# Kernel optimization log

Measured on AMD Instinct MI355X. Metric: run time of the kernel, lower is better.

Reference implementation:

```python
import jax, jax.numpy as jnp
import numpy as np

# Representation config (from init_kwargs): rep1 = rep2 = degrees [0, 1], mult = 32
N = 50000          # nodes
E = 800000         # edges (avg degree 16)
M = 32             # channel multiplicity (rep2.mult)
L_IN = [0, 1]
L_OUT = [0, 1]
D_IN = sum(2 * l + 1 for l in L_IN)    # 4; rep1_cdims = [0, 1, 4]
D_OUT = sum(2 * l + 1 for l in L_OUT)  # 4
OUT_DIMS = np.array([2 * l + 1 for l in L_OUT])  # [1, 3]


def setup_inputs() -> dict:
    key = jax.random.key(0)
    k1, k2, k3, k4 = jax.random.split(key, 4)
    basis = jax.random.normal(k1, (E, D_OUT, D_IN), dtype=jnp.float32)
    edge_weights = jax.random.normal(k2, (E, len(L_OUT), M), dtype=jnp.float32)
    node_features = jax.random.normal(k3, (N, D_IN, M), dtype=jnp.float32)
    U = jax.random.randint(k4, (E,), 0, N)  # edge source node indices
    return {"basis": basis, "edge_weights": edge_weights,
            "node_features": node_features, "U": U}


def reference(basis, edge_weights, node_features, U):
    # matmulStepOne: gather source-node features per edge, contract with the
    # per-edge equivariant basis (block-structured over rep1 degree slices;
    # equivalent to one dense [D_OUT, D_IN] matmul per edge).
    x = node_features[U]                          # [E, D_IN, M] (irregular gather)
    tmp = jnp.einsum('eoi,eim->eom', basis, x)    # [E, D_OUT, M]
    # matmulStepTwo: degree-wise weighted combine — each output degree block
    # (of size 2l+1) is scaled by its per-edge, per-channel radial weight.
    w = jnp.repeat(edge_weights, OUT_DIMS, axis=1, total_repeat_length=D_OUT)  # [E, D_OUT, M]
    return tmp * w
```

## Files before the change

### kernel.cpp

```cpp
#include <hip/hip_runtime.h>


typedef float f4 __attribute__((ext_vector_type(4)));

__global__ __launch_bounds__(256) void equiv_mm_kernel(
    const float* __restrict__ basis,
    const float* __restrict__ ew,
    const float* __restrict__ nf,
    const int*   __restrict__ U,
    float*       __restrict__ out,
    int E)
{
    int gid = blockIdx.x * blockDim.x + threadIdx.x;
    int e = gid >> 3;
    if (e >= E) return;
    int m0 = (gid & 7) << 2;

    int u = U[e];

    const f4* xp = (const f4*)(nf + (size_t)u * 128 + m0);
    f4 x0 = xp[0];
    f4 x1 = xp[8];
    f4 x2 = xp[16];
    f4 x3 = xp[24];

    const f4* bp = (const f4*)(basis + (size_t)e * 16);
    f4 b0 = bp[0], b1 = bp[1], b2 = bp[2], b3 = bp[3];

    const f4* wp = (const f4*)(ew + (size_t)e * 64 + m0);
    f4 w0 = wp[0];
    f4 w1 = wp[8];

    f4* op = (f4*)(out + (size_t)e * 128 + m0);
    op[0]  = (b0.x * x0 + b0.y * x1 + b0.z * x2 + b0.w * x3) * w0;
    op[8]  = (b1.x * x0 + b1.y * x1 + b1.z * x2 + b1.w * x3) * w1;
    op[16] = (b2.x * x0 + b2.y * x1 + b2.z * x2 + b2.w * x3) * w1;
    op[24] = (b3.x * x0 + b3.y * x1 + b3.z * x2 + b3.w * x3) * w1;
}

extern "C" void kernel_launch(void* const* d_in, const int* in_sizes, int n_in,
                              void* d_out, int out_size, void* d_ws, size_t ws_size,
                              hipStream_t stream) {
    const float* basis = (const float*)d_in[0];
    const float* ew    = (const float*)d_in[1];
    const float* nf    = (const float*)d_in[2];
    const int*   U     = (const int*)d_in[3];
    float* out = (float*)d_out;

    int E = in_sizes[0] / 16;
    long long total = (long long)E * 8;
    int block = 256;
    int grid = (int)((total + block - 1) / block);

    equiv_mm_kernel<<<grid, block, 0, stream>>>(basis, ew, nf, U, out, E);
}
```

Before: 158.0 us.

## Process two edges per thread with grid-stride loop and nontemporal streaming

Each thread now handles two consecutive edges, loading both U indices as one int2 and issuing both node-feature gathers together. The grid is capped at 2048 blocks and threads walk the work with a grid-stride loop. Basis, edge-weight and output accesses use nontemporal loads and stores so streamed data does not evict gathered node features from cache. A one-block tail kernel handles an odd edge count. The changes add register pressure and a second launch when E is odd.

```diff
diff --git a/kernel.cpp b/kernel.cpp
--- a/kernel.cpp
+++ b/kernel.cpp
@@ -9,33 +9,69 @@
     const float* __restrict__ nf,
     const int*   __restrict__ U,
     float*       __restrict__ out,
-    int E)
+    int E, int total)
 {
-    int gid = blockIdx.x * blockDim.x + threadIdx.x;
-    int e = gid >> 3;
-    if (e >= E) return;
-    int m0 = (gid & 7) << 2;
+    const int stride = gridDim.x * blockDim.x;
+    for (int gid = blockIdx.x * blockDim.x + threadIdx.x; gid < total; gid += stride) {
+        int p  = gid >> 3;
+        int m0 = (gid & 7) << 2;
+        int e0 = p << 1;
+        int e1 = e0 + 1;
 
+        int2 uu = ((const int2*)U)[p];
+
+        const f4* xp0 = (const f4*)(nf + (size_t)uu.x * 128 + m0);
+        const f4* xp1 = (const f4*)(nf + (size_t)uu.y * 128 + m0);
+        f4 a0 = xp0[0], a1 = xp0[8], a2 = xp0[16], a3 = xp0[24];
+        f4 c0 = xp1[0], c1 = xp1[8], c2 = xp1[16], c3 = xp1[24];
+
+        const f4* bp0 = (const f4*)(basis + (size_t)e0 * 16);
+        f4 b00 = __builtin_nontemporal_load(bp0 + 0);
+        f4 b01 = __builtin_nontemporal_load(bp0 + 1);
+        f4 b02 = __builtin_nontemporal_load(bp0 + 2);
+        f4 b03 = __builtin_nontemporal_load(bp0 + 3);
+        f4 b10 = __builtin_nontemporal_load(bp0 + 4);
+        f4 b11 = __builtin_nontemporal_load(bp0 + 5);
+        f4 b12 = __builtin_nontemporal_load(bp0 + 6);
+        f4 b13 = __builtin_nontemporal_load(bp0 + 7);
+
+        const f4* wp0 = (const f4*)(ew + (size_t)e0 * 64 + m0);
+        f4 w00 = __builtin_nontemporal_load(wp0 + 0);
+        f4 w01 = __builtin_nontemporal_load(wp0 + 8);
+        f4 w10 = __builtin_nontemporal_load(wp0 + 16);
+        f4 w11 = __builtin_nontemporal_load(wp0 + 24);
+
+        f4* op0 = (f4*)(out + (size_t)e0 * 128 + m0);
+        __builtin_nontemporal_store((b00.x*a0 + b00.y*a1 + b00.z*a2 + b00.w*a3) * w00, op0 + 0);
+        __builtin_nontemporal_store((b01.x*a0 + b01.y*a1 + b01.z*a2 + b01.w*a3) * w01, op0 + 8);
+        __builtin_nontemporal_store((b02.x*a0 + b02.y*a1 + b02.z*a2 + b02.w*a3) * w01, op0 + 16);
+        __builtin_nontemporal_store((b03.x*a0 + b03.y*a1 + b03.z*a2 + b03.w*a3) * w01, op0 + 24);
+        f4* op1 = (f4*)(out + (size_t)e1 * 128 + m0);
+        __builtin_nontemporal_store((b10.x*c0 + b10.y*c1 + b10.z*c2 + b10.w*c3) * w10, op1 + 0);
+        __builtin_nontemporal_store((b11.x*c0 + b11.y*c1 + b11.z*c2 + b11.w*c3) * w11, op1 + 8);
+        __builtin_nontemporal_store((b12.x*c0 + b12.y*c1 + b12.z*c2 + b12.w*c3) * w11, op1 + 16);
+        __builtin_nontemporal_store((b13.x*c0 + b13.y*c1 + b13.z*c2 + b13.w*c3) * w11, op1 + 24);
+    }
+}
+
+__global__ void equiv_mm_tail(
+    const float* __restrict__ basis, const float* __restrict__ ew,
+    const float* __restrict__ nf, const int* __restrict__ U,
+    float* __restrict__ out, int e)
+{
+    int m0 = (threadIdx.x & 7) << 2;
     int u = U[e];
-
     const f4* xp = (const f4*)(nf + (size_t)u * 128 + m0);
-    f4 x0 = xp[0];
-    f4 x1 = xp[8];
-    f4 x2 = xp[16];
-    f4 x3 = xp[24];
-
+    f4 a0 = xp[0], a1 = xp[8], a2 = xp[16], a3 = xp[24];
     const f4* bp = (const f4*)(basis + (size_t)e * 16);
     f4 b0 = bp[0], b1 = bp[1], b2 = bp[2], b3 = bp[3];
-
     const f4* wp = (const f4*)(ew + (size_t)e * 64 + m0);
-    f4 w0 = wp[0];
-    f4 w1 = wp[8];
-
+    f4 w0 = wp[0], w1 = wp[8];
     f4* op = (f4*)(out + (size_t)e * 128 + m0);
-    op[0]  = (b0.x * x0 + b0.y * x1 + b0.z * x2 + b0.w * x3) * w0;
-    op[8]  = (b1.x * x0 + b1.y * x1 + b1.z * x2 + b1.w * x3) * w1;
-    op[16] = (b2.x * x0 + b2.y * x1 + b2.z * x2 + b2.w * x3) * w1;
-    op[24] = (b3.x * x0 + b3.y * x1 + b3.z * x2 + b3.w * x3) * w1;
+    op[0]  = (b0.x*a0 + b0.y*a1 + b0.z*a2 + b0.w*a3) * w0;
+    op[8]  = (b1.x*a0 + b1.y*a1 + b1.z*a2 + b1.w*a3) * w1;
+    op[16] = (b2.x*a0 + b2.y*a1 + b2.z*a2 + b2.w*a3) * w1;
+    op[24] = (b3.x*a0 + b3.y*a1 + b3.z*a2 + b3.w*a3) * w1;
 }
 
 extern "C" void kernel_launch(void* const* d_in, const int* in_sizes, int n_in,
@@ -48,9 +84,13 @@
     float* out = (float*)d_out;
 
     int E = in_sizes[0] / 16;
-    long long total = (long long)E * 8;
+    int pairs = E >> 1;
+    int total = pairs * 8;
     int block = 256;
-    int grid = (int)((total + block - 1) / block);
+    int grid = (total + block - 1) / block;
+    if (grid > 2048) grid = 2048;
 
-    equiv_mm_kernel<<<grid, block, 0, stream>>>(basis, ew, nf, U, out, E);
+    equiv_mm_kernel<<<grid, block, 0, stream>>>(basis, ew, nf, U, out, E, total);
+    if (E & 1)
+        equiv_mm_tail<<<1, 8, 0, stream>>>(basis, ew, nf, U, out, E - 1);
 }
```

Result: slower. 169.9 us (+7.6%).
